# Performance work log

Measured on AMD Instinct MI355X. Metric: run time of the kernel, lower is better.

The kernel has to match this reference:

```python
import jax, jax.numpy as jnp
import numpy as np

N_PROD = 500_000   # number of product nodes in the layer (one arity group)
N_EDGES = 4        # padded (power-of-2) children per node
N_SRC = 1_000_001  # rows of node_mars; row 0 is the reserved zero/padding row
B = 128            # batch size


def setup_inputs() -> dict:
    key = jax.random.key(0)
    k1, k2 = jax.random.split(key)
    node_mars = jax.random.normal(k1, (N_SRC, B), dtype=jnp.float32)
    # pyjuice reserves index 0 as a zero row so padded child slots contribute 0
    node_mars = node_mars.at[0].set(0.0)
    element_mars = jnp.zeros((N_PROD + 1, B), dtype=jnp.float32)
    nids = jnp.arange(1, N_PROD + 1, dtype=jnp.int32)  # output slots (0 reserved)
    cids = jax.random.randint(k2, (N_PROD, N_EDGES), 1, N_SRC, dtype=jnp.int32)
    return {"node_mars": node_mars, "element_mars": element_mars,
            "nids": nids, "cids": cids}


def reference(node_mars, element_mars, nids, cids):
    # element_mars[nids] = node_mars[cids].sum(dim=1)
    summed = node_mars[cids].sum(axis=1)          # [N_PROD, B]
    return element_mars.at[nids].set(summed)       # [N_PROD+1, B]
```

## Files before the change

### kernel.cpp

```cpp
#include <hip/hip_runtime.h>


#define B4 32

__global__ __launch_bounds__(256) void prod_layer_kernel(
    const float4* __restrict__ nm,
    const float4* __restrict__ em,
    const int*    __restrict__ nids,
    const int4*   __restrict__ cids,
    float4*       __restrict__ out,
    int n_prod)
{
    int tid   = blockIdx.x * blockDim.x + threadIdx.x;
    int node  = tid >> 5;
    int chunk = tid & 31;
    if (node > n_prod) return;

    if (node == 0) {
        out[chunk] = em[chunk];
        return;
    }

    int p = node - 1;
    int4 c = cids[p];

    float4 a = nm[c.x * B4 + chunk];
    float4 b = nm[c.y * B4 + chunk];
    float4 d = nm[c.z * B4 + chunk];
    float4 e = nm[c.w * B4 + chunk];

    float4 s;
    s.x = (a.x + b.x) + (d.x + e.x);
    s.y = (a.y + b.y) + (d.y + e.y);
    s.z = (a.z + b.z) + (d.z + e.z);
    s.w = (a.w + b.w) + (d.w + e.w);

    out[nids[p] * B4 + chunk] = s;
}

extern "C" void kernel_launch(void* const* d_in, const int* in_sizes, int n_in,
                              void* d_out, int out_size, void* d_ws, size_t ws_size,
                              hipStream_t stream) {
    const float4* nm   = (const float4*)d_in[0];
    const float4* em   = (const float4*)d_in[1];
    const int*    nids = (const int*)d_in[2];
    const int4*   cids = (const int4*)d_in[3];
    float4*       out  = (float4*)d_out;

    const int n_prod = in_sizes[2];
    const long total_threads = (long)(n_prod + 1) * B4;
    const int block = 256;
    const int grid  = (int)((total_threads + block - 1) / block);

    prod_layer_kernel<<<grid, block, 0, stream>>>(nm, em, nids, cids, out, n_prod);
}
```

Baseline: 867.7 us.

## Process 32 nodes per 32-lane group with LDS-staged indices and nontemporal stores

Each 32-lane group now handles 32 product nodes in a loop instead of one node per group. The group loads the cids and nids for its nodes cooperatively into shared memory, then each iteration gathers four child rows and writes the sum with a nontemporal store. This cuts the scalar index loads per node and the number of waves launched, and keeps output writes from polluting cache. In exchange there are far fewer waves to hide gather latency, occupancy is capped through launch bounds, and each group's loop runs serially.

```diff
diff --git a/kernel.cpp b/kernel.cpp
--- a/kernel.cpp
+++ b/kernel.cpp
@@ -1,9 +1,13 @@
 #include <hip/hip_runtime.h>
 
 
-#define B4 32
+#define B4  32
+#define NPG 32
+#define GPB 8
 
-__global__ __launch_bounds__(256) void prod_layer_kernel(
+typedef float fvec4 __attribute__((ext_vector_type(4)));
+
+__global__ __launch_bounds__(256, 4) void prod_layer_kernel(
     const float4* __restrict__ nm,
     const float4* __restrict__ em,
     const int*    __restrict__ nids,
@@ -11,31 +15,47 @@
     float4*       __restrict__ out,
     int n_prod)
 {
-    int tid   = blockIdx.x * blockDim.x + threadIdx.x;
-    int node  = tid >> 5;
-    int chunk = tid & 31;
-    if (node > n_prod) return;
+    __shared__ int4 s_cids[GPB][NPG];
+    __shared__ int  s_dst [GPB][NPG];
 
-    if (node == 0) {
-        out[chunk] = em[chunk];
+    const int grp  = threadIdx.x >> 5;
+    const int lane = threadIdx.x & 31;
+    const int g    = blockIdx.x * GPB + grp;
+
+    const int n_groups = (n_prod + NPG - 1) / NPG;
+
+    if (g >= n_groups) {
+        if (g == n_groups) out[lane] = em[lane];
         return;
     }
 
-    int p = node - 1;
-    int4 c = cids[p];
+    const int pbase = g * NPG;
+    const int cnt   = min(NPG, n_prod - pbase);
 
-    float4 a = nm[c.x * B4 + chunk];
-    float4 b = nm[c.y * B4 + chunk];
-    float4 d = nm[c.z * B4 + chunk];
-    float4 e = nm[c.w * B4 + chunk];
+    if (lane < cnt) {
+        s_cids[grp][lane] = cids[pbase + lane];
+        s_dst [grp][lane] = nids[pbase + lane];
+    }
+    __builtin_amdgcn_wave_barrier();
 
-    float4 s;
-    s.x = (a.x + b.x) + (d.x + e.x);
-    s.y = (a.y + b.y) + (d.y + e.y);
-    s.z = (a.z + b.z) + (d.z + e.z);
-    s.w = (a.w + b.w) + (d.w + e.w);
+    #pragma unroll 4
+    for (int j = 0; j < cnt; ++j) {
+        const int4 c   = s_cids[grp][j];
+        const int  dst = s_dst [grp][j];
 
-    out[nids[p] * B4 + chunk] = s;
+        float4 a = nm[c.x * B4 + lane];
+        float4 b = nm[c.y * B4 + lane];
+        float4 d = nm[c.z * B4 + lane];
+        float4 e = nm[c.w * B4 + lane];
+
+        float4 s;
+        s.x = (a.x + b.x) + (d.x + e.x);
+        s.y = (a.y + b.y) + (d.y + e.y);
+        s.z = (a.z + b.z) + (d.z + e.z);
+        s.w = (a.w + b.w) + (d.w + e.w);
+
+        __builtin_nontemporal_store(*(const fvec4*)&s, (fvec4*)&out[dst * B4 + lane]);
+    }
 }
 
 extern "C" void kernel_launch(void* const* d_in, const int* in_sizes, int n_in,
@@ -47,10 +67,11 @@
     const int4*   cids = (const int4*)d_in[3];
     float4*       out  = (float4*)d_out;
 
-    const int n_prod = in_sizes[2];
-    const long total_threads = (long)(n_prod + 1) * B4;
-    const int block = 256;
-    const int grid  = (int)((total_threads + block - 1) / block);
+    const int n_prod   = in_sizes[2];
+    const int n_groups = (n_prod + NPG - 1) / NPG;
+    const int total_g  = n_groups + 1;
+    const int block    = 256;
+    const int grid     = (total_g + GPB - 1) / GPB;
 
     prod_layer_kernel<<<grid, block, 0, stream>>>(nm, em, nids, cids, out, n_prod);
 }
```

Measured after the change: 874.3 us. No clear change (+0.8%).
